# Performance work log

Measured on AMD Instinct MI355X. Metric: run time of the kernel, lower is better.

## Reference

```python
import jax, jax.numpy as jnp
import numpy as np

BETA = 0.8
THR = 1.0
SLOPE = 25.0  # snntorch surrogate.fast_sigmoid default slope


@jax.custom_vjp
def spike(m):
    # Heaviside fire at threshold; surrogate grad = 1/(slope*|m-thr|+1)^2
    return (m > THR).astype(m.dtype)

def _spike_fwd(m):
    return spike(m), m

def _spike_bwd(m, g):
    d = SLOPE * jnp.abs(m - THR) + 1.0
    return (g / (d * d),)

spike.defvjp(_spike_fwd, _spike_bwd)


def _kaiming(key, out_f, in_f):
    std = np.sqrt(2.0 / in_f)  # kaiming_normal_, fan_in, gain sqrt(2)
    return jax.random.normal(key, (out_f, in_f), dtype=jnp.float32) * std


def setup_inputs() -> dict:
    key = jax.random.key(0)
    kx, k1, k2, k3 = jax.random.split(key, 4)
    T, B, NI, NH, NO = 100, 1024, 512, 256, 3
    return {
        "x": jax.random.normal(kx, (T, B, NI), dtype=jnp.float32),
        "W1": _kaiming(k1, NH, NI), "b1": jnp.zeros((NH,), jnp.float32),
        "W2": _kaiming(k2, NH, NH), "b2": jnp.zeros((NH,), jnp.float32),
        "W3": _kaiming(k3, NO, NH), "b3": jnp.zeros((NO,), jnp.float32),
    }


def _lif(mem_prev, cur):
    # snntorch Leaky, reset_mechanism='subtract': reset based on previous mem,
    # detached (stop_gradient); then fire from the new membrane potential.
    reset = jax.lax.stop_gradient((mem_prev > THR).astype(cur.dtype))
    mem = BETA * mem_prev + cur - reset * THR
    return spike(mem), mem


def reference(x, W1, b1, W2, b2, W3, b3):
    T, B = x.shape[0], x.shape[1]
    NH, NO = W1.shape[0], W3.shape[0]
    mem0 = (jnp.zeros((B, NH), x.dtype), jnp.zeros((B, NH), x.dtype),
            jnp.zeros((B, NO), x.dtype))

    def step(carry, x_t):
        m1, m2, m3 = carry
        s1, m1 = _lif(m1, x_t @ W1.T + b1)
        s2, m2 = _lif(m2, s1 @ W2.T + b2)
        s3, m3 = _lif(m3, s2 @ W3.T + b3)
        return (m1, m2, m3), s3

    (m1, m2, m3), spk_hist = jax.lax.scan(step, mem0, x)
    return spk_hist, m3
```

## Files before the change

kernel.cpp:

```cpp
#include <hip/hip_runtime.h>


typedef unsigned short u16;
typedef unsigned int   u32;

#define THR   128
#define TC    16
#define KB    16
#define MAXNH 256
#define MAXNO 4
#define SPAD  260

__device__ __forceinline__ float bf2f(u16 u){ union{u32 i;float f;}c; c.i=((u32)u)<<16; return c.f; }
__device__ __forceinline__ float ldin(const void*p,size_t e,int bf){
    return bf ? bf2f(((const u16*)p)[e]) : ((const float*)p)[e];
}
__device__ __forceinline__ float4 ldin4(const void*p,size_t e,int bf){
    if(bf){ const ushort4 u=*reinterpret_cast<const ushort4*>((const u16*)p+e);
            return float4{bf2f(u.x),bf2f(u.y),bf2f(u.z),bf2f(u.w)}; }
    return *reinterpret_cast<const float4*>((const float*)p+e);
}

__global__ __launch_bounds__(THR,2)
void snn_f32(const void* __restrict__ x,
             const void* __restrict__ W1, const void* __restrict__ b1,
             const void* __restrict__ W2, const void* __restrict__ b2,
             const void* __restrict__ W3, const void* __restrict__ b3,
             float* __restrict__ out,
             int T,int B,int NI,int NH,int NO)
{
    __shared__ __align__(16) float xs[TC][KB];
    __shared__ __align__(16) float wt[KB][MAXNH+1];
    __shared__ __align__(16) float spk[TC][SPAD];
    __shared__ __align__(16) float w3s[MAXNO][SPAD];
    __shared__ float d3[TC][MAXNO];
    __shared__ int   flg[8];

    const int tid=threadIdx.x, gr=blockIdx.x;
    int* red=(int*)&w3s[0][0];

    {
        const u16* ptab[7]={(const u16*)x,(const u16*)W1,(const u16*)W2,
                            (const u16*)W3,(const u16*)b1,(const u16*)b2,(const u16*)b3};
        int ntab[7];
        ntab[0]=1024; ntab[1]=1024; ntab[2]=1024;
        ntab[3]=(NO*NH>=512)?512:NO*NH;
        ntab[4]=(NH<256)?NH:256; ntab[5]=ntab[4];
        ntab[6]=(NO<MAXNO)?NO:MAXNO;
        for(int ti=0;ti<7;++ti){
            const u16* p=ptab[ti]; const int n=ntab[ti];
            int cnt=0,nz=0;
            for(int i=tid;i<n;i+=THR){ u16 v=p[i]; if(v)++nz;
                float a=fabsf(bf2f(v)); if(a>1e-3f&&a<64.f)++cnt; }
            red[tid]=cnt; __syncthreads();
            for(int s=THR/2;s>0;s>>=1){ if(tid<s) red[tid]+=red[tid+s]; __syncthreads(); }
            int ca=red[0]; __syncthreads();
            red[tid]=nz; __syncthreads();
            for(int s=THR/2;s>0;s>>=1){ if(tid<s) red[tid]+=red[tid+s]; __syncthreads(); }
            if(tid==0){ int na=red[0]; flg[ti]=(na==0)?-1:((ca*5>n*4)?1:0); }
            __syncthreads();
        }
    }
    const int fx =__builtin_amdgcn_readfirstlane(flg[0]==1);
    const int fw1=__builtin_amdgcn_readfirstlane(flg[1]==1);
    const int fw2=__builtin_amdgcn_readfirstlane(flg[2]==1);
    const int fw3=__builtin_amdgcn_readfirstlane(flg[3]==1);

    float bb1[2]={0.f,0.f}, bb2[2]={0.f,0.f};
#pragma unroll
    for(int jj=0;jj<2;++jj){
        const int n=tid+THR*jj;
        if(n<NH){ if(flg[4]>=0) bb1[jj]=ldin(b1,(size_t)n,flg[4]==1);
                  if(flg[5]>=0) bb2[jj]=ldin(b2,(size_t)n,flg[5]==1); }
    }
    float bb3v=0.f;
    if(tid<NO && flg[6]>=0) bb3v=ldin(b3,(size_t)tid,flg[6]==1);
    __syncthreads();

    for(int e=tid;e<MAXNO*MAXNH;e+=THR){
        int o=e>>8,k=e&255;
        w3s[o][k]=(o<NO&&k<NH)? ldin(W3,(size_t)o*NH+k,fw3):0.f;
    }
    for(int e=tid;e<TC*SPAD;e+=THR) (&spk[0][0])[e]=0.f;
    __syncthreads();

    float m1[2]={0.f,0.f}, m2[2]={0.f,0.f}, m3r=0.f;
    float acc[TC][2];

    for(int t0=0;t0<T;t0+=TC){
        const int tc=(T-t0<TC)?(T-t0):TC;

#pragma unroll
        for(int tt=0;tt<TC;++tt){ acc[tt][0]=0.f; acc[tt][1]=0.f; }

        for(int kb=0;kb<NI;kb+=KB){
            if(tid<TC*(KB/4)){
                int tt=tid>>2, kq=(tid&3)*4;
                float4 v={0.f,0.f,0.f,0.f};
                if(tt<tc && kb+kq+3<NI)
                    v=ldin4(x,((size_t)(t0+tt)*B+gr)*NI+kb+kq,fx);
                else if(tt<tc){
                    float tmp[4];
#pragma unroll
                    for(int j=0;j<4;++j)
                        tmp[j]=(kb+kq+j<NI)?ldin(x,((size_t)(t0+tt)*B+gr)*NI+kb+kq+j,fx):0.f;
                    v=float4{tmp[0],tmp[1],tmp[2],tmp[3]};
                }
                *reinterpret_cast<float4*>(&xs[tt][kq])=v;
            }
            for(int e=tid;e<KB*64;e+=THR){
                int kq=(e&3)*4, n=e>>2;
                float4 v={0.f,0.f,0.f,0.f};
                if(n<NH && kb+kq+3<NI) v=ldin4(W1,(size_t)n*NI+kb+kq,fw1);
                else if(n<NH){
                    float tmp[4];
#pragma unroll
                    for(int j=0;j<4;++j)
                        tmp[j]=(kb+kq+j<NI)?ldin(W1,(size_t)n*NI+kb+kq+j,fw1):0.f;
                    v=float4{tmp[0],tmp[1],tmp[2],tmp[3]};
                }
                wt[kq+0][n]=v.x; wt[kq+1][n]=v.y; wt[kq+2][n]=v.z; wt[kq+3][n]=v.w;
            }
            __syncthreads();
#pragma unroll
            for(int q=0;q<KB/4;++q){
                const float wa0=wt[q*4+0][tid],     wa1=wt[q*4+1][tid];
                const float wa2=wt[q*4+2][tid],     wa3=wt[q*4+3][tid];
                const float wb0=wt[q*4+0][tid+THR], wb1=wt[q*4+1][tid+THR];
                const float wb2=wt[q*4+2][tid+THR], wb3=wt[q*4+3][tid+THR];
#pragma unroll
                for(int tt=0;tt<TC;++tt){
                    const float4 xv=*reinterpret_cast<const float4*>(&xs[tt][q*4]);
                    float a=acc[tt][0];
                    a=fmaf(wa0,xv.x,a); a=fmaf(wa1,xv.y,a);
                    a=fmaf(wa2,xv.z,a); a=fmaf(wa3,xv.w,a);
                    acc[tt][0]=a;
                    float b=acc[tt][1];
                    b=fmaf(wb0,xv.x,b); b=fmaf(wb1,xv.y,b);
                    b=fmaf(wb2,xv.z,b); b=fmaf(wb3,xv.w,b);
                    acc[tt][1]=b;
                }
            }
            __syncthreads();
        }
#pragma unroll
        for(int jj=0;jj<2;++jj){
            const int n=tid+THR*jj;
            if(n<NH){
#pragma unroll
                for(int tt=0;tt<TC;++tt){
                    if(tt<tc){
                        float cur=__fadd_rn(acc[tt][jj],bb1[jj]);
                        float rst=(m1[jj]>1.0f)?1.0f:0.0f;
                        m1[jj]=__fsub_rn(__fadd_rn(__fmul_rn(0.8f,m1[jj]),cur),rst);
                        spk[tt][n]=(m1[jj]>1.0f)?1.0f:0.0f;
                    }
                }
            }
        }
        __syncthreads();

#pragma unroll
        for(int tt=0;tt<TC;++tt){ acc[tt][0]=0.f; acc[tt][1]=0.f; }

        for(int kb=0;kb<NH;kb+=KB){
            for(int e=tid;e<KB*64;e+=THR){
                int kq=(e&3)*4, n=e>>2;
                float4 v={0.f,0.f,0.f,0.f};
                if(n<NH && kb+kq+3<NH) v=ldin4(W2,(size_t)n*NH+kb+kq,fw2);
                else if(n<NH){
                    float tmp[4];
#pragma unroll
                    for(int j=0;j<4;++j)
                        tmp[j]=(kb+kq+j<NH)?ldin(W2,(size_t)n*NH+kb+kq+j,fw2):0.f;
                    v=float4{tmp[0],tmp[1],tmp[2],tmp[3]};
                }
                wt[kq+0][n]=v.x; wt[kq+1][n]=v.y; wt[kq+2][n]=v.z; wt[kq+3][n]=v.w;
            }
            __syncthreads();
#pragma unroll
            for(int q=0;q<KB/4;++q){
                const float wa0=wt[q*4+0][tid],     wa1=wt[q*4+1][tid];
                const float wa2=wt[q*4+2][tid],     wa3=wt[q*4+3][tid];
                const float wb0=wt[q*4+0][tid+THR], wb1=wt[q*4+1][tid+THR];
                const float wb2=wt[q*4+2][tid+THR], wb3=wt[q*4+3][tid+THR];
#pragma unroll
                for(int tt=0;tt<TC;++tt){
                    const float4 sv=*reinterpret_cast<const float4*>(&spk[tt][kb+q*4]);
                    float a=acc[tt][0];
                    a=fmaf(wa0,sv.x,a); a=fmaf(wa1,sv.y,a);
                    a=fmaf(wa2,sv.z,a); a=fmaf(wa3,sv.w,a);
                    acc[tt][0]=a;
                    float b=acc[tt][1];
                    b=fmaf(wb0,sv.x,b); b=fmaf(wb1,sv.y,b);
                    b=fmaf(wb2,sv.z,b); b=fmaf(wb3,sv.w,b);
                    acc[tt][1]=b;
                }
            }
            __syncthreads();
        }
#pragma unroll
        for(int jj=0;jj<2;++jj){
            const int n=tid+THR*jj;
            if(n<NH){
#pragma unroll
                for(int tt=0;tt<TC;++tt){
                    if(tt<tc){
                        float cur=__fadd_rn(acc[tt][jj],bb2[jj]);
                        float rst=(m2[jj]>1.0f)?1.0f:0.0f;
                        m2[jj]=__fsub_rn(__fadd_rn(__fmul_rn(0.8f,m2[jj]),cur),rst);
                        spk[tt][n]=(m2[jj]>1.0f)?1.0f:0.0f;
                    }
                }
            }
        }
        __syncthreads();

        if(tid<TC*NO){
            const int tt=tid/NO, o=tid%NO;
            if(tt<tc){
                float a3=0.f;
                int k=0;
                for(; k+3<NH; k+=4){
                    const float4 sv=*reinterpret_cast<const float4*>(&spk[tt][k]);
                    const float4 wv=*reinterpret_cast<const float4*>(&w3s[o][k]);
                    a3=fmaf(wv.x,sv.x,a3); a3=fmaf(wv.y,sv.y,a3);
                    a3=fmaf(wv.z,sv.z,a3); a3=fmaf(wv.w,sv.w,a3);
                }
                for(; k<NH; ++k) a3=fmaf(w3s[o][k],spk[tt][k],a3);
                d3[tt][o]=a3;
            }
        }
        __syncthreads();
        if(tid<NO){
            const int o=tid;
            for(int tt=0;tt<tc;++tt){
                float cur=__fadd_rn(d3[tt][o],bb3v);
                float rst=(m3r>1.0f)?1.0f:0.0f;
                m3r=__fsub_rn(__fadd_rn(__fmul_rn(0.8f,m3r),cur),rst);
                out[((size_t)(t0+tt)*B+gr)*(size_t)NO+o]=(m3r>1.0f)?1.0f:0.0f;
            }
        }
        __syncthreads();
    }

    if(tid<NO)
        out[(size_t)T*B*NO+(size_t)gr*NO+tid]=m3r;
}

extern "C" void kernel_launch(void* const* d_in, const int* in_sizes, int n_in,
                              void* d_out, int out_size, void* d_ws, size_t ws_size,
                              hipStream_t stream)
{
    const void* x  = d_in[0];
    const void* W1 = d_in[1];
    const void* b1 = d_in[2];
    const void* W2 = d_in[3];
    const void* b2 = d_in[4];
    const void* W3 = d_in[5];
    const void* b3 = d_in[6];

    int NH = in_sizes[2];              if (NH <= 0 || NH > MAXNH) NH = 256;
    int NI = in_sizes[1] / NH;         if (NI <= 0) NI = 512;
    int NO = in_sizes[6];              if (NO <= 0 || NO > MAXNO) NO = 3;
    long TB = (long)in_sizes[0] / NI;
    long BN = (long)out_size / NO;
    int B = (int)(BN - TB);            if (B <= 0) B = 1024;
    int T = (int)(TB / B);             if (T <= 0) T = 1;

    snn_f32<<<dim3(B), dim3(THR), 0, stream>>>(
        x, W1, b1, W2, b2, W3, b3, (float*)d_out, T, B, NI, NH, NO);
}
```

Measured before the change: 1.363 ms.

## Load weights straight into registers, widen x tile, drop LDS weight staging

The W1 and W2 weight tiles are no longer staged through shared memory. Each thread now loads its own two weight rows straight from global memory (L2-resident) into registers in chunks of 16. The x tile is widened to 64 k-values, and the layer-2 loop drops its per-chunk barriers, so there are far fewer __syncthreads and no LDS transposed stores. Launch bounds are raised to three blocks per SM to get more occupancy. The cost is more redundant global and L2 traffic, since each block rereads all the weights with row-strided per-thread loads, plus higher register pressure.

```diff
diff --git a/kernel.cpp b/kernel.cpp
--- a/kernel.cpp
+++ b/kernel.cpp
@@ -6,7 +6,8 @@
 
 #define THR   128
 #define TC    16
-#define KB    16
+#define KBX   64
+#define KW    16
 #define MAXNH 256
 #define MAXNO 4
 #define SPAD  260
@@ -20,8 +21,20 @@
             return float4{bf2f(u.x),bf2f(u.y),bf2f(u.z),bf2f(u.w)}; }
     return *reinterpret_cast<const float4*>((const float*)p+e);
 }
-
-__global__ __launch_bounds__(THR,2)
+__device__ __forceinline__ float4 ldw4(const void*W,int n,int NR,int K,int k,int bf){
+    float4 v={0.f,0.f,0.f,0.f};
+    if(n<NR){
+        if(k+3<K) v=ldin4(W,(size_t)n*K+k,bf);
+        else{
+#pragma unroll
+            for(int j=0;j<4;++j)
+                ((float*)&v)[j]=(k+j<K)?ldin(W,(size_t)n*K+k+j,bf):0.f;
+        }
+    }
+    return v;
+}
+
+__global__ __launch_bounds__(THR,3)
 void snn_f32(const void* __restrict__ x,
              const void* __restrict__ W1, const void* __restrict__ b1,
              const void* __restrict__ W2, const void* __restrict__ b2,
@@ -29,8 +42,7 @@
              float* __restrict__ out,
              int T,int B,int NI,int NH,int NO)
 {
-    __shared__ __align__(16) float xs[TC][KB];
-    __shared__ __align__(16) float wt[KB][MAXNH+1];
+    __shared__ __align__(16) float xs[TC][KBX];
     __shared__ __align__(16) float spk[TC][SPAD];
     __shared__ __align__(16) float w3s[MAXNO][SPAD];
     __shared__ float d3[TC][MAXNO];
@@ -66,6 +78,8 @@
     const int fw2=__builtin_amdgcn_readfirstlane(flg[2]==1);
     const int fw3=__builtin_amdgcn_readfirstlane(flg[3]==1);
 
+    const int n0=tid, n1=tid+THR;
+
     float bb1[2]={0.f,0.f}, bb2[2]={0.f,0.f};
 #pragma unroll
     for(int jj=0;jj<2;++jj){
@@ -86,6 +100,7 @@
 
     float m1[2]={0.f,0.f}, m2[2]={0.f,0.f}, m3r=0.f;
     float acc[TC][2];
+    float wr0[KW], wr1[KW];
 
     for(int t0=0;t0<T;t0+=TC){
         const int tc=(T-t0<TC)?(T-t0):TC;
@@ -93,52 +108,46 @@
 #pragma unroll
         for(int tt=0;tt<TC;++tt){ acc[tt][0]=0.f; acc[tt][1]=0.f; }
 
-        for(int kb=0;kb<NI;kb+=KB){
-            if(tid<TC*(KB/4)){
-                int tt=tid>>2, kq=(tid&3)*4;
+        for(int kb=0;kb<NI;kb+=KBX){
+            for(int e=tid;e<TC*(KBX/4);e+=THR){
+                const int tt=e/(KBX/4), kq=(e%(KBX/4))*4;
                 float4 v={0.f,0.f,0.f,0.f};
-                if(tt<tc && kb+kq+3<NI)
-                    v=ldin4(x,((size_t)(t0+tt)*B+gr)*NI+kb+kq,fx);
-                else if(tt<tc){
-                    float tmp[4];
-#pragma unroll
-                    for(int j=0;j<4;++j)
-                        tmp[j]=(kb+kq+j<NI)?ldin(x,((size_t)(t0+tt)*B+gr)*NI+kb+kq+j,fx):0.f;
-                    v=float4{tmp[0],tmp[1],tmp[2],tmp[3]};
+                if(tt<tc){
+                    const size_t base=((size_t)(t0+tt)*B+gr)*(size_t)NI;
+                    if(kb+kq+3<NI) v=ldin4(x,base+kb+kq,fx);
+                    else{
+#pragma unroll
+                        for(int j=0;j<4;++j)
+                            ((float*)&v)[j]=(kb+kq+j<NI)?ldin(x,base+kb+kq+j,fx):0.f;
+                    }
                 }
                 *reinterpret_cast<float4*>(&xs[tt][kq])=v;
             }
-            for(int e=tid;e<KB*64;e+=THR){
-                int kq=(e&3)*4, n=e>>2;
-                float4 v={0.f,0.f,0.f,0.f};
-                if(n<NH && kb+kq+3<NI) v=ldin4(W1,(size_t)n*NI+kb+kq,fw1);
-                else if(n<NH){
-                    float tmp[4];
-#pragma unroll
-                    for(int j=0;j<4;++j)
-                        tmp[j]=(kb+kq+j<NI)?ldin(W1,(size_t)n*NI+kb+kq+j,fw1):0.f;
-                    v=float4{tmp[0],tmp[1],tmp[2],tmp[3]};
-                }
-                wt[kq+0][n]=v.x; wt[kq+1][n]=v.y; wt[kq+2][n]=v.z; wt[kq+3][n]=v.w;
-            }
             __syncthreads();
-#pragma unroll
-            for(int q=0;q<KB/4;++q){
-                const float wa0=wt[q*4+0][tid],     wa1=wt[q*4+1][tid];
-                const float wa2=wt[q*4+2][tid],     wa3=wt[q*4+3][tid];
-                const float wb0=wt[q*4+0][tid+THR], wb1=wt[q*4+1][tid+THR];
-                const float wb2=wt[q*4+2][tid+THR], wb3=wt[q*4+3][tid+THR];
-#pragma unroll
-                for(int tt=0;tt<TC;++tt){
-                    const float4 xv=*reinterpret_cast<const float4*>(&xs[tt][q*4]);
-                    float a=acc[tt][0];
-                    a=fmaf(wa0,xv.x,a); a=fmaf(wa1,xv.y,a);
-                    a=fmaf(wa2,xv.z,a); a=fmaf(wa3,xv.w,a);
-                    acc[tt][0]=a;
-                    float b=acc[tt][1];
-                    b=fmaf(wb0,xv.x,b); b=fmaf(wb1,xv.y,b);
-                    b=fmaf(wb2,xv.z,b); b=fmaf(wb3,xv.w,b);
-                    acc[tt][1]=b;
+
+            for(int kw=0;kw<KBX && kb+kw<NI;kw+=KW){
+#pragma unroll
+                for(int q=0;q<KW/4;++q){
+                    const int k=kb+kw+q*4;
+                    const float4 a=ldw4(W1,n0,NH,NI,k,fw1);
+                    const float4 b=ldw4(W1,n1,NH,NI,k,fw1);
+                    wr0[q*4+0]=a.x; wr0[q*4+1]=a.y; wr0[q*4+2]=a.z; wr0[q*4+3]=a.w;
+                    wr1[q*4+0]=b.x; wr1[q*4+1]=b.y; wr1[q*4+2]=b.z; wr1[q*4+3]=b.w;
+                }
+#pragma unroll
+                for(int q=0;q<KW/4;++q){
+#pragma unroll
+                    for(int tt=0;tt<TC;++tt){
+                        const float4 xv=*reinterpret_cast<const float4*>(&xs[tt][kw+q*4]);
+                        float a=acc[tt][0];
+                        a=fmaf(wr0[q*4+0],xv.x,a); a=fmaf(wr0[q*4+1],xv.y,a);
+                        a=fmaf(wr0[q*4+2],xv.z,a); a=fmaf(wr0[q*4+3],xv.w,a);
+                        acc[tt][0]=a;
+                        float b=acc[tt][1];
+                        b=fmaf(wr1[q*4+0],xv.x,b); b=fmaf(wr1[q*4+1],xv.y,b);
+                        b=fmaf(wr1[q*4+2],xv.z,b); b=fmaf(wr1[q*4+3],xv.w,b);
+                        acc[tt][1]=b;
+                    }
                 }
             }
             __syncthreads();
@@ -163,42 +172,33 @@
 #pragma unroll
         for(int tt=0;tt<TC;++tt){ acc[tt][0]=0.f; acc[tt][1]=0.f; }
 
-        for(int kb=0;kb<NH;kb+=KB){
-            for(int e=tid;e<KB*64;e+=THR){
-                int kq=(e&3)*4, n=e>>2;
-                float4 v={0.f,0.f,0.f,0.f};
-                if(n<NH && kb+kq+3<NH) v=ldin4(W2,(size_t)n*NH+kb+kq,fw2);
-                else if(n<NH){
-                    float tmp[4];
-#pragma unroll
-                    for(int j=0;j<4;++j)
-                        tmp[j]=(kb+kq+j<NH)?ldin(W2,(size_t)n*NH+kb+kq+j,fw2):0.f;
-                    v=float4{tmp[0],tmp[1],tmp[2],tmp[3]};
-                }
-                wt[kq+0][n]=v.x; wt[kq+1][n]=v.y; wt[kq+2][n]=v.z; wt[kq+3][n]=v.w;
-            }
-            __syncthreads();
-#pragma unroll
-            for(int q=0;q<KB/4;++q){
-                const float wa0=wt[q*4+0][tid],     wa1=wt[q*4+1][tid];
-                const float wa2=wt[q*4+2][tid],     wa3=wt[q*4+3][tid];
-                const float wb0=wt[q*4+0][tid+THR], wb1=wt[q*4+1][tid+THR];
-                const float wb2=wt[q*4+2][tid+THR], wb3=wt[q*4+3][tid+THR];
+        for(int kw=0;kw<NH;kw+=KW){
+#pragma unroll
+            for(int q=0;q<KW/4;++q){
+                const int k=kw+q*4;
+                const float4 a=ldw4(W2,n0,NH,NH,k,fw2);
+                const float4 b=ldw4(W2,n1,NH,NH,k,fw2);
+                wr0[q*4+0]=a.x; wr0[q*4+1]=a.y; wr0[q*4+2]=a.z; wr0[q*4+3]=a.w;
+                wr1[q*4+0]=b.x; wr1[q*4+1]=b.y; wr1[q*4+2]=b.z; wr1[q*4+3]=b.w;
+            }
+#pragma unroll
+            for(int q=0;q<KW/4;++q){
 #pragma unroll
                 for(int tt=0;tt<TC;++tt){
-                    const float4 sv=*reinterpret_cast<const float4*>(&spk[tt][kb+q*4]);
+                    const float4 sv=*reinterpret_cast<const float4*>(&spk[tt][kw+q*4]);
                     float a=acc[tt][0];
-                    a=fmaf(wa0,sv.x,a); a=fmaf(wa1,sv.y,a);
-                    a=fmaf(wa2,sv.z,a); a=fmaf(wa3,sv.w,a);
+                    a=fmaf(wr0[q*4+0],sv.x,a); a=fmaf(wr0[q*4+1],sv.y,a);
+                    a=fmaf(wr0[q*4+2],sv.z,a); a=fmaf(wr0[q*4+3],sv.w,a);
                     acc[tt][0]=a;
                     float b=acc[tt][1];
-                    b=fmaf(wb0,sv.x,b); b=fmaf(wb1,sv.y,b);
-                    b=fmaf(wb2,sv.z,b); b=fmaf(wb3,sv.w,b);
+                    b=fmaf(wr1[q*4+0],sv.x,b); b=fmaf(wr1[q*4+1],sv.y,b);
+                    b=fmaf(wr1[q*4+2],sv.z,b); b=fmaf(wr1[q*4+3],sv.w,b);
                     acc[tt][1]=b;
                 }
             }
-            __syncthreads();
-        }
+        }
+        __syncthreads();
+
 #pragma unroll
         for(int jj=0;jj<2;++jj){
             const int n=tid+THR*jj;
```

Result: slower. 1.677 ms, median of 2 (+23.0%).
